# Optimization experiments

Hardware: AMD Instinct MI355X
Metric: run time of the kernel (lower is better)

## Reference

```python
import jax, jax.numpy as jnp
import numpy as np

N = 100000
E = 1600000
D = 128
EPS = 1e-5


def setup_inputs() -> dict:
    key = jax.random.key(0)
    ks = jax.random.split(key, 8)
    s = 1.0 / np.sqrt(D)
    feats = jax.random.normal(ks[0], (N, D), dtype=jnp.float32)
    src = jax.random.randint(ks[1], (E,), 0, N, dtype=jnp.int32)
    dst = jax.random.randint(ks[2], (E,), 0, N, dtype=jnp.int32)
    W_gcn = jax.random.normal(ks[3], (D, D), dtype=jnp.float32) * s
    b_gcn = jnp.zeros((D,), dtype=jnp.float32)
    W_res = jax.random.normal(ks[4], (D, D), dtype=jnp.float32) * s
    b_res = jnp.zeros((D,), dtype=jnp.float32)
    g1 = jnp.ones((D,), dtype=jnp.float32)
    be1 = jnp.zeros((D,), dtype=jnp.float32)
    g2 = jnp.ones((D,), dtype=jnp.float32)
    be2 = jnp.zeros((D,), dtype=jnp.float32)
    return {"feats": feats, "W_gcn": W_gcn, "b_gcn": b_gcn, "W_res": W_res,
            "b_res": b_res, "g1": g1, "be1": be1, "g2": g2, "be2": be2,
            "src": src, "dst": dst}


def _batchnorm(x, gamma, beta):
    # BatchNorm1d, training mode: biased batch stats over the node dim
    mu = jnp.mean(x, axis=0)
    var = jnp.var(x, axis=0)
    return gamma * (x - mu) * jax.lax.rsqrt(var + EPS) + beta


def reference(feats, W_gcn, b_gcn, W_res, b_res, g1, be1, g2, be2, src, dst):
    n = feats.shape[0]
    # GraphConv(norm='none'): sum-aggregate neighbor feats then linear (in<=out)
    agg = jax.ops.segment_sum(feats[src], dst, num_segments=n)  # [N, D]
    h = jax.nn.relu(agg @ W_gcn + b_gcn)
    # dgllife GCNLayer internal residual: activation(Linear(feats))
    res = jax.nn.relu(feats @ W_res + b_res)
    h = _batchnorm(h + res, g1, be1)
    # outer ResidualGCNLayer: Identity residual (in_feats==out_feats) + BN
    out = _batchnorm(h + feats, g2, be2)
    return out
```

## Files before the change

### kernel.cpp

```cpp
#include <hip/hip_runtime.h>
#include <hip/hip_bf16.h>
#include <stdint.h>

#define NN 100000
#define EE 1600000
#define DD 128
#define EPSV 1e-5f
#define WWIN 128
#define NB 782
#define NCLS 8
#define NSEG (NB * NCLS)
#define ITEMS (EE / 4)
#define ITEMS_PER_CLS (ITEMS / NCLS)
#define SORTCAP 4096

typedef __attribute__((ext_vector_type(8))) short short8;
typedef __attribute__((ext_vector_type(4))) float floatx4;
typedef unsigned short u16;

union S8 { short8 v; short s[8]; unsigned short u[8]; };

__device__ __forceinline__ float bf2f(u16 u) {
    return __uint_as_float(((unsigned int)u) << 16);
}
__device__ __forceinline__ u16 f2bf(float f) {
    unsigned int x = __float_as_uint(f);
    x += 0x7FFFu + ((x >> 16) & 1u);
    return (u16)(x >> 16);
}


__global__ void k_detect(const float* __restrict__ f, int* __restrict__ flag) {
    __shared__ int cnt;
    if (threadIdx.x == 0) cnt = 0;
    __syncthreads();
    const float v = fabsf(f[threadIdx.x]);
    if (v > 1e-3f && v < 1e3f) atomicAdd(&cnt, 1);
    __syncthreads();
    if (threadIdx.x == 0) *flag = (cnt >= 128) ? 1 : 0;
}

__global__ __launch_bounds__(256) void k_convert(
    const int* __restrict__ flag, const float* __restrict__ ff,
    const float* __restrict__ Wg, const float* __restrict__ Wr,
    const float* __restrict__ bg, const float* __restrict__ br,
    const float* __restrict__ g1, const float* __restrict__ g2,
    const float* __restrict__ be2,
    u16* __restrict__ fc, u16* __restrict__ pc)
{
    if (*flag == 0) return;
    const int bx = blockIdx.x;
    if (bx < 131) {
        const int i = bx * 256 + threadIdx.x;
        if (i >= 33408) return;
        float v;
        if (i < 16384)      v = Wg[i];
        else if (i < 32768) v = Wr[i - 16384];
        else {
            const int j = i - 32768;
            const int a = j >> 7, o = j & 127;
            v = (a == 0) ? bg[o] : (a == 1) ? br[o] : (a == 2) ? g1[o]
              : (a == 3) ? g2[o] : be2[o];
        }
        pc[i] = f2bf(v);
        return;
    }
    const int bid = bx - 131;
    const size_t P = (size_t)NN * (DD / 4);
    for (size_t i = (size_t)bid * 256 + threadIdx.x; i < P;
         i += (size_t)1024 * 256) {
        const float4 v = *(const float4*)(ff + 4 * i);
        uint2 o;
        o.x = (unsigned int)f2bf(v.x) | ((unsigned int)f2bf(v.y) << 16);
        o.y = (unsigned int)f2bf(v.z) | ((unsigned int)f2bf(v.w) << 16);
        *(uint2*)(fc + 4 * i) = o;
    }
}

__global__ __launch_bounds__(256) void k_hist2(
    const int* __restrict__ dst, int* __restrict__ cnt)
{
    __shared__ int lc[NB];
    const int cls  = blockIdx.x & 7;
    const int blk  = blockIdx.x >> 3;
    const int nblk = gridDim.x >> 3;
    const int it0  = cls * ITEMS_PER_CLS;
    const int it1  = it0 + ITEMS_PER_CLS;
    for (int i = threadIdx.x; i < NB; i += 256) lc[i] = 0;
    __syncthreads();
    const int4* __restrict__ dst4 = (const int4*)dst;
    for (int it = it0 + blk * blockDim.x + threadIdx.x; it < it1;
         it += nblk * blockDim.x) {
        const int4 d = dst4[it];
        atomicAdd(&lc[d.x >> 7], 1);
        atomicAdd(&lc[d.y >> 7], 1);
        atomicAdd(&lc[d.z >> 7], 1);
        atomicAdd(&lc[d.w >> 7], 1);
    }
    __syncthreads();
    for (int i = threadIdx.x; i < NB; i += 256) {
        const int v = lc[i];
        if (v) atomicAdd(&cnt[i * NCLS + cls], v);
    }
}

__global__ __launch_bounds__(1024) void k_scanseg(
    const int* __restrict__ cnt, int* __restrict__ off,
    int* __restrict__ cursor)
{
    const int tx = threadIdx.x;
    const int lane = tx & 63, w = tx >> 6;
    __shared__ int wsum[16];
    __shared__ int carry;
    if (tx == 0) carry = 0;
    __syncthreads();
    for (int base = 0; base < NSEG; base += 1024) {
        const int i = base + tx;
        const int v = (i < NSEG) ? cnt[i] : 0;
        int incl = v;
#pragma unroll
        for (int d = 1; d < 64; d <<= 1) {
            const int n = __shfl_up(incl, d, 64);
            if (lane >= d) incl += n;
        }
        if (lane == 63) wsum[w] = incl;
        __syncthreads();
        if (tx < 16) {
            int s = wsum[tx];
#pragma unroll
            for (int d = 1; d < 16; d <<= 1) {
                const int n = __shfl_up(s, d, 16);
                if ((tx & 15) >= d) s += n;
            }
            wsum[tx] = s;
        }
        __syncthreads();
        const int c = carry;
        const int woff = (w == 0) ? 0 : wsum[w - 1];
        if (i < NSEG) {
            const int excl = c + woff + incl - v;
            off[i] = excl;
            cursor[i] = excl;
        }
        __syncthreads();
        if (tx == 0) carry = c + wsum[15];
        __syncthreads();
    }
    if (tx == 0) off[NSEG] = carry;
}

__global__ __launch_bounds__(256) void k_bin(
    const int* __restrict__ src, const int* __restrict__ dst,
    int* __restrict__ cursor, unsigned int* __restrict__ arena)
{
    __shared__ int lc[NB], lb[NB];
    const int cls  = blockIdx.x & 7;
    const int blk  = blockIdx.x >> 3;
    const int nblk = gridDim.x >> 3;
    const int it0  = cls * ITEMS_PER_CLS;
    const int it1  = it0 + ITEMS_PER_CLS;
    const int4* __restrict__ dst4 = (const int4*)dst;
    const int4* __restrict__ src4 = (const int4*)src;
    for (int i = threadIdx.x; i < NB; i += 256) lc[i] = 0;
    __syncthreads();
    for (int it = it0 + blk * blockDim.x + threadIdx.x; it < it1;
         it += nblk * blockDim.x) {
        const int4 d = dst4[it];
        atomicAdd(&lc[d.x >> 7], 1);
        atomicAdd(&lc[d.y >> 7], 1);
        atomicAdd(&lc[d.z >> 7], 1);
        atomicAdd(&lc[d.w >> 7], 1);
    }
    __syncthreads();
    for (int i = threadIdx.x; i < NB; i += 256) {
        const int v = lc[i];
        lb[i] = v ? atomicAdd(&cursor[i * NCLS + cls], v) : 0;
    }
    __syncthreads();
    for (int i = threadIdx.x; i < NB; i += 256) lc[i] = 0;
    __syncthreads();
    for (int it = it0 + blk * blockDim.x + threadIdx.x; it < it1;
         it += nblk * blockDim.x) {
        const int4 d = dst4[it];
        const int4 s = src4[it];
        int wv, p;
        wv = d.x >> 7; p = lb[wv] + atomicAdd(&lc[wv], 1);
        arena[p] = ((unsigned int)(d.x & 127) << 17) | (unsigned int)s.x;
        wv = d.y >> 7; p = lb[wv] + atomicAdd(&lc[wv], 1);
        arena[p] = ((unsigned int)(d.y & 127) << 17) | (unsigned int)s.y;
        wv = d.z >> 7; p = lb[wv] + atomicAdd(&lc[wv], 1);
        arena[p] = ((unsigned int)(d.z & 127) << 17) | (unsigned int)s.z;
        wv = d.w >> 7; p = lb[wv] + atomicAdd(&lc[wv], 1);
        arena[p] = ((unsigned int)(d.w & 127) << 17) | (unsigned int)s.w;
    }
}

__global__ __launch_bounds__(256) void k_winsort(
    unsigned int* __restrict__ arena, const int* __restrict__ off,
    int* __restrict__ row_st)
{
    __shared__ unsigned int buf[SORTCAP];
    __shared__ int cnt[WWIN], pref[WWIN], cur[WWIN];
    const int tx = threadIdx.x;
    const int b = blockIdx.x;
    const int s0 = off[b * NCLS];
    const int s1 = off[b * NCLS + NCLS];
    int len = s1 - s0;
    if (len > SORTCAP) len = SORTCAP;
    if (tx < WWIN) cnt[tx] = 0;
    __syncthreads();
    for (int i = tx; i < len; i += 256) {
        const unsigned int p = arena[s0 + i];
        buf[i] = p;
        atomicAdd(&cnt[p >> 17], 1);
    }
    __syncthreads();
    if (tx < WWIN) pref[tx] = cnt[tx];
    __syncthreads();
    for (int d = 1; d < WWIN; d <<= 1) {
        int v = 0;
        if (tx < WWIN && tx >= d) v = pref[tx - d];
        __syncthreads();
        if (tx < WWIN) pref[tx] += v;
        __syncthreads();
    }
    if (tx < WWIN) {
        const int excl = pref[tx] - cnt[tx];
        cur[tx] = excl;
        const int node = b * WWIN + tx;
        if (node < NN) row_st[node] = s0 + excl;
    }
    if (b == NB - 1 && tx == 0) row_st[NN] = EE;
    __syncthreads();
    for (int i = tx; i < len; i += 256) {
        const unsigned int p = buf[i];
        const int pos = atomicAdd(&cur[p >> 17], 1);
        arena[s0 + pos] = p & 0x1FFFFu;
    }
}

__global__ __launch_bounds__(256, 8) void k_gather(
    const int* __restrict__ flag,
    const u16* __restrict__ feats_raw, const u16* __restrict__ feats_c,
    const int* __restrict__ edge_s, const int* __restrict__ row_st,
    u16* __restrict__ aggb)
{
    const u16* __restrict__ F = (*flag != 0) ? feats_c : feats_raw;
    const int lane = threadIdx.x & 63;
    const int l16  = lane & 15;
    const int gb   = lane & 48;
    const int wave = (blockIdx.x * blockDim.x + threadIdx.x) >> 6;
    const int nw   = (gridDim.x * blockDim.x) >> 6;

    for (int n0 = wave * 4; n0 < NN; n0 += nw * 4) {
        const int node = n0 + (lane >> 4);
        const int rs   = row_st[node];
        const int deg  = row_st[node + 1] - rs;
        float a0 = 0.f, a1 = 0.f, a2 = 0.f, a3 = 0.f;
        float a4 = 0.f, a5 = 0.f, a6 = 0.f, a7 = 0.f;
        for (int ebase = 0; ebase < deg; ebase += 16) {
            const int rem = deg - ebase;
            const int nb  = rem < 16 ? rem : 16;
            int il = 0;
            if (l16 < nb) il = edge_s[rs + ebase + l16];
            int j = 0;
            for (; j + 8 <= nb; j += 8) {
                uint4 vv[8];
#pragma unroll
                for (int q = 0; q < 8; ++q) {
                    const int s = __shfl(il, gb + j + q, 64);
                    vv[q] = *(const uint4*)(F + (size_t)s * DD + l16 * 8);
                }
#pragma unroll
                for (int q = 0; q < 8; ++q) {
                    a0 += bf2f((u16)(vv[q].x & 0xFFFFu));
                    a1 += bf2f((u16)(vv[q].x >> 16));
                    a2 += bf2f((u16)(vv[q].y & 0xFFFFu));
                    a3 += bf2f((u16)(vv[q].y >> 16));
                    a4 += bf2f((u16)(vv[q].z & 0xFFFFu));
                    a5 += bf2f((u16)(vv[q].z >> 16));
                    a6 += bf2f((u16)(vv[q].w & 0xFFFFu));
                    a7 += bf2f((u16)(vv[q].w >> 16));
                }
            }
            for (; j + 4 <= nb; j += 4) {
                uint4 vv[4];
#pragma unroll
                for (int q = 0; q < 4; ++q) {
                    const int s = __shfl(il, gb + j + q, 64);
                    vv[q] = *(const uint4*)(F + (size_t)s * DD + l16 * 8);
                }
#pragma unroll
                for (int q = 0; q < 4; ++q) {
                    a0 += bf2f((u16)(vv[q].x & 0xFFFFu));
                    a1 += bf2f((u16)(vv[q].x >> 16));
                    a2 += bf2f((u16)(vv[q].y & 0xFFFFu));
                    a3 += bf2f((u16)(vv[q].y >> 16));
                    a4 += bf2f((u16)(vv[q].z & 0xFFFFu));
                    a5 += bf2f((u16)(vv[q].z >> 16));
                    a6 += bf2f((u16)(vv[q].w & 0xFFFFu));
                    a7 += bf2f((u16)(vv[q].w >> 16));
                }
            }
            for (; j < nb; ++j) {
                const int s = __shfl(il, gb + j, 64);
                const uint4 v = *(const uint4*)(F + (size_t)s * DD + l16 * 8);
                a0 += bf2f((u16)(v.x & 0xFFFFu));
                a1 += bf2f((u16)(v.x >> 16));
                a2 += bf2f((u16)(v.y & 0xFFFFu));
                a3 += bf2f((u16)(v.y >> 16));
                a4 += bf2f((u16)(v.z & 0xFFFFu));
                a5 += bf2f((u16)(v.z >> 16));
                a6 += bf2f((u16)(v.w & 0xFFFFu));
                a7 += bf2f((u16)(v.w >> 16));
            }
        }
        uint4 o;
        o.x = (unsigned int)f2bf(a0) | ((unsigned int)f2bf(a1) << 16);
        o.y = (unsigned int)f2bf(a2) | ((unsigned int)f2bf(a3) << 16);
        o.z = (unsigned int)f2bf(a4) | ((unsigned int)f2bf(a5) << 16);
        o.w = (unsigned int)f2bf(a6) | ((unsigned int)f2bf(a7) << 16);
        *(uint4*)(aggb + (size_t)node * DD + l16 * 8) = o;
    }
}

__global__ __launch_bounds__(256) void k_gemm(
    const int* __restrict__ flag,
    const u16* __restrict__ aggb,
    const u16* __restrict__ feats_raw, const u16* __restrict__ feats_c,
    const u16* __restrict__ Wg_raw, const u16* __restrict__ bg_raw,
    const u16* __restrict__ Wr_raw, const u16* __restrict__ br_raw,
    const u16* __restrict__ pc,
    u16* __restrict__ t_out, float* __restrict__ stats)
{
    const bool f32 = (*flag != 0);
    const u16* __restrict__ F  = f32 ? feats_c     : feats_raw;
    const u16* __restrict__ Wg = f32 ? pc          : Wg_raw;
    const u16* __restrict__ Wr = f32 ? pc + 16384  : Wr_raw;
    const u16* __restrict__ bg = f32 ? pc + 32768  : bg_raw;
    const u16* __restrict__ br = f32 ? pc + 32896  : br_raw;

    const int lane = threadIdx.x & 63;
    const int wv   = threadIdx.x >> 6;
    const int l15  = lane & 15;
    const int quad = lane >> 4;
    const int c0 = wv * 16 + l15;
    const int c1 = 64 + wv * 16 + l15;

    S8 fg0[4], fg1[4], fr0[4], fr1[4];
#pragma unroll
    for (int kb = 0; kb < 4; ++kb) {
        const int kr = kb * 32 + quad * 8;
#pragma unroll
        for (int j = 0; j < 8; ++j) {
            fg0[kb].u[j] = Wg[(size_t)(kr + j) * DD + c0];
            fg1[kb].u[j] = Wg[(size_t)(kr + j) * DD + c1];
            fr0[kb].u[j] = Wr[(size_t)(kr + j) * DD + c0];
            fr1[kb].u[j] = Wr[(size_t)(kr + j) * DD + c1];
        }
    }
    const float bgc0 = bf2f(bg[c0]), bgc1 = bf2f(bg[c1]);
    const float brc0 = bf2f(br[c0]), brc1 = bf2f(br[c1]);

    float s_t0 = 0.f, s_t1 = 0.f, s_tt0 = 0.f, s_tt1 = 0.f;
    float s_f0 = 0.f, s_f1 = 0.f, s_ff0 = 0.f, s_ff1 = 0.f;
    float s_tf0 = 0.f, s_tf1 = 0.f;

    for (int tile = blockIdx.x; tile < NN / 16; tile += gridDim.x) {
        const int row0 = tile * 16;
        const int arow = row0 + l15;
        floatx4 ag0 = {0.f,0.f,0.f,0.f}, ag1 = {0.f,0.f,0.f,0.f};
        floatx4 ar0 = {0.f,0.f,0.f,0.f}, ar1 = {0.f,0.f,0.f,0.f};
#pragma unroll
        for (int kb = 0; kb < 4; ++kb) {
            const int kbase = kb * 32 + quad * 8;
            S8 av, ff;
            av.v = *(const short8*)(aggb + (size_t)arow * DD + kbase);
            ff.v = *(const short8*)(F    + (size_t)arow * DD + kbase);
            ag0 = __builtin_amdgcn_mfma_f32_16x16x32_bf16(av.v, fg0[kb].v, ag0, 0, 0, 0);
            ag1 = __builtin_amdgcn_mfma_f32_16x16x32_bf16(av.v, fg1[kb].v, ag1, 0, 0, 0);
            ar0 = __builtin_amdgcn_mfma_f32_16x16x32_bf16(ff.v, fr0[kb].v, ar0, 0, 0, 0);
            ar1 = __builtin_amdgcn_mfma_f32_16x16x32_bf16(ff.v, fr1[kb].v, ar1, 0, 0, 0);
        }
#pragma unroll
        for (int r = 0; r < 4; ++r) {
            const int row = row0 + quad * 4 + r;
            const u16 tb0 = f2bf(fmaxf(ag0[r] + bgc0, 0.f) + fmaxf(ar0[r] + brc0, 0.f));
            const u16 tb1 = f2bf(fmaxf(ag1[r] + bgc1, 0.f) + fmaxf(ar1[r] + brc1, 0.f));
            t_out[(size_t)row * DD + c0] = tb0;
            t_out[(size_t)row * DD + c1] = tb1;
            const float t0 = bf2f(tb0), t1 = bf2f(tb1);
            const float fv0 = bf2f(F[(size_t)row * DD + c0]);
            const float fv1 = bf2f(F[(size_t)row * DD + c1]);
            s_t0  += t0;        s_t1  += t1;
            s_tt0 += t0 * t0;   s_tt1 += t1 * t1;
            s_f0  += fv0;       s_f1  += fv1;
            s_ff0 += fv0 * fv0; s_ff1 += fv1 * fv1;
            s_tf0 += t0 * fv0;  s_tf1 += t1 * fv1;
        }
    }

#define QRED(x) x += __shfl_xor(x, 16, 64); x += __shfl_xor(x, 32, 64);
    QRED(s_t0)  QRED(s_t1)  QRED(s_tt0) QRED(s_tt1)
    QRED(s_f0)  QRED(s_f1)  QRED(s_ff0) QRED(s_ff1)
    QRED(s_tf0) QRED(s_tf1)
#undef QRED
    if (quad == 0) {
        unsafeAtomicAdd(&stats[0 * DD + c0], s_t0);
        unsafeAtomicAdd(&stats[0 * DD + c1], s_t1);
        unsafeAtomicAdd(&stats[1 * DD + c0], s_tt0);
        unsafeAtomicAdd(&stats[1 * DD + c1], s_tt1);
        unsafeAtomicAdd(&stats[2 * DD + c0], s_f0);
        unsafeAtomicAdd(&stats[2 * DD + c1], s_f1);
        unsafeAtomicAdd(&stats[3 * DD + c0], s_ff0);
        unsafeAtomicAdd(&stats[3 * DD + c1], s_ff1);
        unsafeAtomicAdd(&stats[4 * DD + c0], s_tf0);
        unsafeAtomicAdd(&stats[4 * DD + c1], s_tf1);
    }
}

__global__ __launch_bounds__(256) void k_final(
    const int* __restrict__ flag,
    const u16* __restrict__ t,
    const u16* __restrict__ feats_raw, const u16* __restrict__ feats_c,
    const u16* __restrict__ g1_raw, const u16* __restrict__ g2_raw,
    const u16* __restrict__ be2_raw, const u16* __restrict__ pc,
    const float* __restrict__ stats,
    void* __restrict__ out)
{
    const bool f32 = (*flag != 0);
    const u16* __restrict__ F   = f32 ? feats_c    : feats_raw;
    const u16* __restrict__ g1  = f32 ? pc + 33024 : g1_raw;
    const u16* __restrict__ g2  = f32 ? pc + 33152 : g2_raw;
    const u16* __restrict__ be2 = f32 ? pc + 33280 : be2_raw;

    __shared__ float sA[DD], sB[DD], sG[DD];
    if (threadIdx.x < DD) {
        const int c = threadIdx.x;
        const float invN = 1.0f / (float)NN;
        const float St  = stats[c],          Stt = stats[DD + c];
        const float Sf  = stats[2 * DD + c], Sff = stats[3 * DD + c];
        const float Stf = stats[4 * DD + c];
        const float mu1  = St * invN;
        const float vart = fmaxf(Stt * invN - mu1 * mu1, 0.f);
        const float muf  = Sf * invN;
        const float varf = fmaxf(Sff * invN - muf * muf, 0.f);
        const float cov  = Stf * invN - mu1 * muf;
        const float r1   = rsqrtf(vart + EPSV);
        const float a1   = bf2f(g1[c]) * r1;
        const float var2 = fmaxf(a1 * a1 * vart + 2.f * a1 * cov + varf, 0.f);
        const float r2   = rsqrtf(var2 + EPSV);
        const float g2r2 = bf2f(g2[c]) * r2;
        sA[c] = g2r2 * a1;
        sB[c] = g2r2;
        sG[c] = bf2f(be2[c]) - g2r2 * (a1 * mu1 + muf);
    }
    __syncthreads();

    float* outf = (float*)out;
    u16*   outb = (u16*)out;
    const size_t P = (size_t)NN * (DD / 4);
    for (size_t i = (size_t)blockIdx.x * blockDim.x + threadIdx.x; i < P;
         i += (size_t)gridDim.x * blockDim.x) {
        const int c = ((int)(i & 31)) * 4;
        const uint2 tv = *(const uint2*)(t + 4 * i);
        const uint2 fv = *(const uint2*)(F + 4 * i);
        const float o0 = sA[c]     * bf2f((u16)(tv.x & 0xFFFFu))
                       + sB[c]     * bf2f((u16)(fv.x & 0xFFFFu)) + sG[c];
        const float o1 = sA[c + 1] * bf2f((u16)(tv.x >> 16))
                       + sB[c + 1] * bf2f((u16)(fv.x >> 16)) + sG[c + 1];
        const float o2 = sA[c + 2] * bf2f((u16)(tv.y & 0xFFFFu))
                       + sB[c + 2] * bf2f((u16)(fv.y & 0xFFFFu)) + sG[c + 2];
        const float o3 = sA[c + 3] * bf2f((u16)(tv.y >> 16))
                       + sB[c + 3] * bf2f((u16)(fv.y >> 16)) + sG[c + 3];
        if (f32) {
            float4 o; o.x = o0; o.y = o1; o.z = o2; o.w = o3;
            *(float4*)(outf + 4 * i) = o;
        } else {
            uint2 ov;
            ov.x = (unsigned int)f2bf(o0) | ((unsigned int)f2bf(o1) << 16);
            ov.y = (unsigned int)f2bf(o2) | ((unsigned int)f2bf(o3) << 16);
            *(uint2*)(outb + 4 * i) = ov;
        }
    }
}

extern "C" void kernel_launch(void* const* d_in, const int* in_sizes, int n_in,
                              void* d_out, int out_size, void* d_ws, size_t ws_size,
                              hipStream_t stream) {
    const u16* feats = (const u16*)d_in[0];
    const u16* Wg    = (const u16*)d_in[1];
    const u16* bg    = (const u16*)d_in[2];
    const u16* Wr    = (const u16*)d_in[3];
    const u16* br    = (const u16*)d_in[4];
    const u16* g1    = (const u16*)d_in[5];
    const u16* g2    = (const u16*)d_in[7];
    const u16* be2   = (const u16*)d_in[8];
    const int* src = (const int*)d_in[9];
    const int* dst = (const int*)d_in[10];

    char* ws = (char*)d_ws;
    u16*          aggb    = (u16*)  ws;
    u16*          t       = (u16*)  (ws + 25600000);
    u16*          feats_c = (u16*)  (ws + 51200000);
    u16*          pc      = (u16*)  (ws + 76800000);
    float*        stats   = (float*)(ws + 76866816);
    int*          flag    = (int*)  (ws + 76869376);
    int*          cnt     = (int*)  (ws + 76869632);
    int*          off     = (int*)  (ws + 76894656);
    int*          cursor  = (int*)  (ws + 76919684);
    int*          row_st  = (int*)  (ws + 76944708);
    unsigned int* arena   = (unsigned int*)(ws + 77344712);

    hipMemsetAsync(cnt,   0, NSEG * sizeof(int), stream);
    hipMemsetAsync(stats, 0, 5 * DD * sizeof(float), stream);

    k_detect<<<1, 256, 0, stream>>>((const float*)d_in[0], flag);
    k_convert<<<1155, 256, 0, stream>>>(flag, (const float*)d_in[0],
        (const float*)d_in[1], (const float*)d_in[3], (const float*)d_in[2],
        (const float*)d_in[4], (const float*)d_in[5], (const float*)d_in[7],
        (const float*)d_in[8], feats_c, pc);

    k_hist2  <<<256, 256, 0, stream>>>(dst, cnt);
    k_scanseg<<<1, 1024, 0, stream>>>(cnt, off, cursor);
    k_bin    <<<256, 256, 0, stream>>>(src, dst, cursor, arena);
    k_winsort<<<NB, 256, 0, stream>>>(arena, off, row_st);

    k_gather<<<2048, 256, 0, stream>>>(flag, feats, feats_c, (const int*)arena, row_st, aggb);
    k_gemm  <<<1024, 256, 0, stream>>>(flag, aggb, feats, feats_c, Wg, bg, Wr, br, pc, t, stats);
    k_final <<<2048, 256, 0, stream>>>(flag, t, feats, feats_c, g1, g2, be2, pc, stats, d_out);
}
```

Measured before the change: 305.1 us.

## Fuse window sort with gather and fold memsets, detect, and scan into neighbors

Merges the per-window sort into the gather kernel so each block sorts its edges into shared memory and aggregates its 128 nodes directly. The separate row_st array and the write-back of sorted indices are dropped. The memsets and flag detection move into k_convert, and the segment scan runs in the last-finishing hist block via an atomic done counter. This cuts several launches and one global round trip of the arena, but gather parallelism is now limited to 782 blocks with large shared memory, which may lower occupancy.

```diff
diff --git a/kernel.cpp b/kernel.cpp
--- a/kernel.cpp
+++ b/kernel.cpp
@@ -30,28 +30,40 @@
 }
 
 
-__global__ void k_detect(const float* __restrict__ f, int* __restrict__ flag) {
-    __shared__ int cnt;
-    if (threadIdx.x == 0) cnt = 0;
-    __syncthreads();
-    const float v = fabsf(f[threadIdx.x]);
-    if (v > 1e-3f && v < 1e3f) atomicAdd(&cnt, 1);
-    __syncthreads();
-    if (threadIdx.x == 0) *flag = (cnt >= 128) ? 1 : 0;
-}
-
 __global__ __launch_bounds__(256) void k_convert(
-    const int* __restrict__ flag, const float* __restrict__ ff,
+    const float* __restrict__ ff,
     const float* __restrict__ Wg, const float* __restrict__ Wr,
     const float* __restrict__ bg, const float* __restrict__ br,
     const float* __restrict__ g1, const float* __restrict__ g2,
     const float* __restrict__ be2,
-    u16* __restrict__ fc, u16* __restrict__ pc)
-{
-    if (*flag == 0) return;
+    u16* __restrict__ fc, u16* __restrict__ pc,
+    int* __restrict__ flag, int* __restrict__ done,
+    int* __restrict__ cnt, float* __restrict__ stats)
+{
     const int bx = blockIdx.x;
-    if (bx < 131) {
-        const int i = bx * 256 + threadIdx.x;
+    const int tx = threadIdx.x;
+    if (bx < 27) {
+        const int idx = bx * 256 + tx;
+        if (idx < 5 * DD) stats[idx] = 0.f;
+        else {
+            const int j = idx - 5 * DD;
+            if (j < NSEG) cnt[j] = 0;
+            else if (j == NSEG) *done = 0;
+        }
+        return;
+    }
+    __shared__ int dc;
+    if (tx == 0) dc = 0;
+    __syncthreads();
+    const float dv = fabsf(ff[tx]);
+    if (dv > 1e-3f && dv < 1e3f) atomicAdd(&dc, 1);
+    __syncthreads();
+    const int myflag = (dc >= 128) ? 1 : 0;
+    if (bx == 27 && tx == 0) *flag = myflag;
+    if (!myflag) return;
+
+    if (bx < 158) {
+        const int i = (bx - 27) * 256 + tx;
         if (i >= 33408) return;
         float v;
         if (i < 16384)      v = Wg[i];
@@ -65,10 +77,9 @@
         pc[i] = f2bf(v);
         return;
     }
-    const int bid = bx - 131;
+    const int bid = bx - 158;
     const size_t P = (size_t)NN * (DD / 4);
-    for (size_t i = (size_t)bid * 256 + threadIdx.x; i < P;
-         i += (size_t)1024 * 256) {
+    for (size_t i = (size_t)bid * 256 + tx; i < P; i += (size_t)1024 * 256) {
         const float4 v = *(const float4*)(ff + 4 * i);
         uint2 o;
         o.x = (unsigned int)f2bf(v.x) | ((unsigned int)f2bf(v.y) << 16);
@@ -78,19 +89,20 @@
 }
 
 __global__ __launch_bounds__(256) void k_hist2(
-    const int* __restrict__ dst, int* __restrict__ cnt)
+    const int* __restrict__ dst, int* __restrict__ cnt,
+    int* __restrict__ done, int* __restrict__ off, int* __restrict__ cursor)
 {
     __shared__ int lc[NB];
+    const int tx   = threadIdx.x;
     const int cls  = blockIdx.x & 7;
     const int blk  = blockIdx.x >> 3;
     const int nblk = gridDim.x >> 3;
     const int it0  = cls * ITEMS_PER_CLS;
     const int it1  = it0 + ITEMS_PER_CLS;
-    for (int i = threadIdx.x; i < NB; i += 256) lc[i] = 0;
+    for (int i = tx; i < NB; i += 256) lc[i] = 0;
     __syncthreads();
     const int4* __restrict__ dst4 = (const int4*)dst;
-    for (int it = it0 + blk * blockDim.x + threadIdx.x; it < it1;
-         it += nblk * blockDim.x) {
+    for (int it = it0 + blk * 256 + tx; it < it1; it += nblk * 256) {
         const int4 d = dst4[it];
         atomicAdd(&lc[d.x >> 7], 1);
         atomicAdd(&lc[d.y >> 7], 1);
@@ -98,25 +110,26 @@
         atomicAdd(&lc[d.w >> 7], 1);
     }
     __syncthreads();
-    for (int i = threadIdx.x; i < NB; i += 256) {
+    for (int i = tx; i < NB; i += 256) {
         const int v = lc[i];
         if (v) atomicAdd(&cnt[i * NCLS + cls], v);
     }
-}
-
-__global__ __launch_bounds__(1024) void k_scanseg(
-    const int* __restrict__ cnt, int* __restrict__ off,
-    int* __restrict__ cursor)
-{
-    const int tx = threadIdx.x;
+    __threadfence();
+    __shared__ int last;
+    if (tx == 0) last = (atomicAdd(done, 1) == (int)gridDim.x - 1) ? 1 : 0;
+    __syncthreads();
+    if (!last) return;
+
     const int lane = tx & 63, w = tx >> 6;
-    __shared__ int wsum[16];
+    __shared__ int wsum[4];
     __shared__ int carry;
     if (tx == 0) carry = 0;
     __syncthreads();
-    for (int base = 0; base < NSEG; base += 1024) {
+    for (int base = 0; base < NSEG; base += 256) {
         const int i = base + tx;
-        const int v = (i < NSEG) ? cnt[i] : 0;
+        int v = 0;
+        if (i < NSEG)
+            v = __hip_atomic_load(&cnt[i], __ATOMIC_RELAXED, __HIP_MEMORY_SCOPE_AGENT);
         int incl = v;
 #pragma unroll
         for (int d = 1; d < 64; d <<= 1) {
@@ -125,14 +138,10 @@
         }
         if (lane == 63) wsum[w] = incl;
         __syncthreads();
-        if (tx < 16) {
-            int s = wsum[tx];
-#pragma unroll
-            for (int d = 1; d < 16; d <<= 1) {
-                const int n = __shfl_up(s, d, 16);
-                if ((tx & 15) >= d) s += n;
-            }
-            wsum[tx] = s;
+        if (tx == 0) {
+            int s = 0;
+#pragma unroll
+            for (int k = 0; k < 4; ++k) { s += wsum[k]; wsum[k] = s; }
         }
         __syncthreads();
         const int c = carry;
@@ -143,7 +152,7 @@
             cursor[i] = excl;
         }
         __syncthreads();
-        if (tx == 0) carry = c + wsum[15];
+        if (tx == 0) carry = c + wsum[3];
         __syncthreads();
     }
     if (tx == 0) off[NSEG] = carry;
@@ -195,27 +204,30 @@
     }
 }
 
-__global__ __launch_bounds__(256) void k_winsort(
-    unsigned int* __restrict__ arena, const int* __restrict__ off,
-    int* __restrict__ row_st)
+__global__ __launch_bounds__(256) void k_sortgather(
+    const int* __restrict__ flag,
+    const u16* __restrict__ feats_raw, const u16* __restrict__ feats_c,
+    const unsigned int* __restrict__ arena, const int* __restrict__ off,
+    u16* __restrict__ aggb)
 {
     __shared__ unsigned int buf[SORTCAP];
-    __shared__ int cnt[WWIN], pref[WWIN], cur[WWIN];
+    __shared__ int sorted[SORTCAP];
+    __shared__ int cnt_[WWIN], pref[WWIN], cur[WWIN];
+    const u16* __restrict__ F = (*flag != 0) ? feats_c : feats_raw;
     const int tx = threadIdx.x;
-    const int b = blockIdx.x;
+    const int b  = blockIdx.x;
     const int s0 = off[b * NCLS];
-    const int s1 = off[b * NCLS + NCLS];
-    int len = s1 - s0;
+    int len = off[b * NCLS + NCLS] - s0;
     if (len > SORTCAP) len = SORTCAP;
-    if (tx < WWIN) cnt[tx] = 0;
+    if (tx < WWIN) cnt_[tx] = 0;
     __syncthreads();
     for (int i = tx; i < len; i += 256) {
         const unsigned int p = arena[s0 + i];
         buf[i] = p;
-        atomicAdd(&cnt[p >> 17], 1);
-    }
-    __syncthreads();
-    if (tx < WWIN) pref[tx] = cnt[tx];
+        atomicAdd(&cnt_[p >> 17], 1);
+    }
+    __syncthreads();
+    if (tx < WWIN) pref[tx] = cnt_[tx];
     __syncthreads();
     for (int d = 1; d < WWIN; d <<= 1) {
         int v = 0;
@@ -224,103 +236,65 @@
         if (tx < WWIN) pref[tx] += v;
         __syncthreads();
     }
-    if (tx < WWIN) {
-        const int excl = pref[tx] - cnt[tx];
-        cur[tx] = excl;
-        const int node = b * WWIN + tx;
-        if (node < NN) row_st[node] = s0 + excl;
-    }
-    if (b == NB - 1 && tx == 0) row_st[NN] = EE;
+    if (tx < WWIN) cur[tx] = pref[tx] - cnt_[tx];
     __syncthreads();
     for (int i = tx; i < len; i += 256) {
         const unsigned int p = buf[i];
         const int pos = atomicAdd(&cur[p >> 17], 1);
-        arena[s0 + pos] = p & 0x1FFFFu;
-    }
-}
-
-__global__ __launch_bounds__(256, 8) void k_gather(
-    const int* __restrict__ flag,
-    const u16* __restrict__ feats_raw, const u16* __restrict__ feats_c,
-    const int* __restrict__ edge_s, const int* __restrict__ row_st,
-    u16* __restrict__ aggb)
-{
-    const u16* __restrict__ F = (*flag != 0) ? feats_c : feats_raw;
-    const int lane = threadIdx.x & 63;
+        sorted[pos] = (int)(p & 0x1FFFFu);
+    }
+    __syncthreads();
+
+    const int lane = tx & 63;
     const int l16  = lane & 15;
-    const int gb   = lane & 48;
-    const int wave = (blockIdx.x * blockDim.x + threadIdx.x) >> 6;
-    const int nw   = (gridDim.x * blockDim.x) >> 6;
-
-    for (int n0 = wave * 4; n0 < NN; n0 += nw * 4) {
-        const int node = n0 + (lane >> 4);
-        const int rs   = row_st[node];
-        const int deg  = row_st[node + 1] - rs;
+    const int wv   = tx >> 6;
+    for (int it = 0; it < 8; ++it) {
+        const int nloc = wv * 32 + it * 4 + (lane >> 4);
+        const int node = b * WWIN + nloc;
+        const int deg  = cnt_[nloc];
+        const int rs   = pref[nloc] - deg;
         float a0 = 0.f, a1 = 0.f, a2 = 0.f, a3 = 0.f;
         float a4 = 0.f, a5 = 0.f, a6 = 0.f, a7 = 0.f;
-        for (int ebase = 0; ebase < deg; ebase += 16) {
-            const int rem = deg - ebase;
-            const int nb  = rem < 16 ? rem : 16;
-            int il = 0;
-            if (l16 < nb) il = edge_s[rs + ebase + l16];
-            int j = 0;
-            for (; j + 8 <= nb; j += 8) {
-                uint4 vv[8];
-#pragma unroll
-                for (int q = 0; q < 8; ++q) {
-                    const int s = __shfl(il, gb + j + q, 64);
-                    vv[q] = *(const uint4*)(F + (size_t)s * DD + l16 * 8);
-                }
-#pragma unroll
-                for (int q = 0; q < 8; ++q) {
-                    a0 += bf2f((u16)(vv[q].x & 0xFFFFu));
-                    a1 += bf2f((u16)(vv[q].x >> 16));
-                    a2 += bf2f((u16)(vv[q].y & 0xFFFFu));
-                    a3 += bf2f((u16)(vv[q].y >> 16));
-                    a4 += bf2f((u16)(vv[q].z & 0xFFFFu));
-                    a5 += bf2f((u16)(vv[q].z >> 16));
-                    a6 += bf2f((u16)(vv[q].w & 0xFFFFu));
-                    a7 += bf2f((u16)(vv[q].w >> 16));
-                }
+        int j = 0;
+        for (; j + 8 <= deg; j += 8) {
+            uint4 vv[8];
+#pragma unroll
+            for (int q = 0; q < 8; ++q) {
+                const int s = sorted[rs + j + q];
+                vv[q] = *(const uint4*)(F + (size_t)s * DD + l16 * 8);
             }
-            for (; j + 4 <= nb; j += 4) {
-                uint4 vv[4];
-#pragma unroll
-                for (int q = 0; q < 4; ++q) {
-                    const int s = __shfl(il, gb + j + q, 64);
-                    vv[q] = *(const uint4*)(F + (size_t)s * DD + l16 * 8);
-                }
-#pragma unroll
-                for (int q = 0; q < 4; ++q) {
-                    a0 += bf2f((u16)(vv[q].x & 0xFFFFu));
-                    a1 += bf2f((u16)(vv[q].x >> 16));
-                    a2 += bf2f((u16)(vv[q].y & 0xFFFFu));
-                    a3 += bf2f((u16)(vv[q].y >> 16));
-                    a4 += bf2f((u16)(vv[q].z & 0xFFFFu));
-                    a5 += bf2f((u16)(vv[q].z >> 16));
-                    a6 += bf2f((u16)(vv[q].w & 0xFFFFu));
-                    a7 += bf2f((u16)(vv[q].w >> 16));
-                }
+#pragma unroll
+            for (int q = 0; q < 8; ++q) {
+                a0 += bf2f((u16)(vv[q].x & 0xFFFFu));
+                a1 += bf2f((u16)(vv[q].x >> 16));
+                a2 += bf2f((u16)(vv[q].y & 0xFFFFu));
+                a3 += bf2f((u16)(vv[q].y >> 16));
+                a4 += bf2f((u16)(vv[q].z & 0xFFFFu));
+                a5 += bf2f((u16)(vv[q].z >> 16));
+                a6 += bf2f((u16)(vv[q].w & 0xFFFFu));
+                a7 += bf2f((u16)(vv[q].w >> 16));
             }
-            for (; j < nb; ++j) {
-                const int s = __shfl(il, gb + j, 64);
-                const uint4 v = *(const uint4*)(F + (size_t)s * DD + l16 * 8);
-                a0 += bf2f((u16)(v.x & 0xFFFFu));
-                a1 += bf2f((u16)(v.x >> 16));
-                a2 += bf2f((u16)(v.y & 0xFFFFu));
-                a3 += bf2f((u16)(v.y >> 16));
-                a4 += bf2f((u16)(v.z & 0xFFFFu));
-                a5 += bf2f((u16)(v.z >> 16));
-                a6 += bf2f((u16)(v.w & 0xFFFFu));
-                a7 += bf2f((u16)(v.w >> 16));
-            }
-        }
-        uint4 o;
-        o.x = (unsigned int)f2bf(a0) | ((unsigned int)f2bf(a1) << 16);
-        o.y = (unsigned int)f2bf(a2) | ((unsigned int)f2bf(a3) << 16);
-        o.z = (unsigned int)f2bf(a4) | ((unsigned int)f2bf(a5) << 16);
-        o.w = (unsigned int)f2bf(a6) | ((unsigned int)f2bf(a7) << 16);
-        *(uint4*)(aggb + (size_t)node * DD + l16 * 8) = o;
+        }
+        for (; j < deg; ++j) {
+            const int s = sorted[rs + j];
+            const uint4 v = *(const uint4*)(F + (size_t)s * DD + l16 * 8);
+            a0 += bf2f((u16)(v.x & 0xFFFFu));
+            a1 += bf2f((u16)(v.x >> 16));
+            a2 += bf2f((u16)(v.y & 0xFFFFu));
+            a3 += bf2f((u16)(v.y >> 16));
+            a4 += bf2f((u16)(v.z & 0xFFFFu));
+            a5 += bf2f((u16)(v.z >> 16));
+            a6 += bf2f((u16)(v.w & 0xFFFFu));
+            a7 += bf2f((u16)(v.w >> 16));
+        }
+        if (node < NN) {
+            uint4 o;
+            o.x = (unsigned int)f2bf(a0) | ((unsigned int)f2bf(a1) << 16);
+            o.y = (unsigned int)f2bf(a2) | ((unsigned int)f2bf(a3) << 16);
+            o.z = (unsigned int)f2bf(a4) | ((unsigned int)f2bf(a5) << 16);
+            o.w = (unsigned int)f2bf(a6) | ((unsigned int)f2bf(a7) << 16);
+            *(uint4*)(aggb + (size_t)node * DD + l16 * 8) = o;
+        }
     }
 }
 
@@ -506,27 +480,20 @@
     u16*          pc      = (u16*)  (ws + 76800000);
     float*        stats   = (float*)(ws + 76866816);
     int*          flag    = (int*)  (ws + 76869376);
+    int*          done    = (int*)  (ws + 76869380);
     int*          cnt     = (int*)  (ws + 76869632);
     int*          off     = (int*)  (ws + 76894656);
     int*          cursor  = (int*)  (ws + 76919684);
-    int*          row_st  = (int*)  (ws + 76944708);
     unsigned int* arena   = (unsigned int*)(ws + 77344712);
 
-    hipMemsetAsync(cnt,   0, NSEG * sizeof(int), stream);
-    hipMemsetAsync(stats, 0, 5 * DD * sizeof(float), stream);
-
-    k_detect<<<1, 256, 0, stream>>>((const float*)d_in[0], flag);
-    k_convert<<<1155, 256, 0, stream>>>(flag, (const float*)d_in[0],
+    k_convert<<<1182, 256, 0, stream>>>((const float*)d_in[0],
         (const float*)d_in[1], (const float*)d_in[3], (const float*)d_in[2],
         (const float*)d_in[4], (const float*)d_in[5], (const float*)d_in[7],
-        (const float*)d_in[8], feats_c, pc);
-
-    k_hist2  <<<256, 256, 0, stream>>>(dst, cnt);
-    k_scanseg<<<1, 1024, 0, stream>>>(cnt, off, cursor);
-    k_bin    <<<256, 256, 0, stream>>>(src, dst, cursor, arena);
-    k_winsort<<<NB, 256, 0, stream>>>(arena, off, row_st);
-
-    k_gather<<<2048, 256, 0, stream>>>(flag, feats, feats_c, (const int*)arena, row_st, aggb);
-    k_gemm  <<<1024, 256, 0, stream>>>(flag, aggb, feats, feats_c, Wg, bg, Wr, br, pc, t, stats);
-    k_final <<<2048, 256, 0, stream>>>(flag, t, feats, feats_c, g1, g2, be2, pc, stats, d_out);
-}
+        (const float*)d_in[8], feats_c, pc, flag, done, cnt, stats);
+
+    k_hist2<<<256, 256, 0, stream>>>(dst, cnt, done, off, cursor);
+    k_bin  <<<256, 256, 0, stream>>>(src, dst, cursor, arena);
+    k_sortgather<<<NB, 256, 0, stream>>>(flag, feats, feats_c, arena, off, aggb);
+    k_gemm <<<1024, 256, 0, stream>>>(flag, aggb, feats, feats_c, Wg, bg, Wr, br, pc, t, stats);
+    k_final<<<2048, 256, 0, stream>>>(flag, t, feats, feats_c, g1, g2, be2, pc, stats, d_out);
+}
```

After: 313.8 us. 1.03x slower.
